# Kernel tuning notes

Hardware: AMD Instinct MI355X
Metric: run time of the kernel (lower is better)

## Reference

```python
import jax, jax.numpy as jnp
from jax import lax
import numpy as np

STRIDE = 2
EXT_PAD = (2, 2)  # computed in __init__: (total_pad - inter_pad)//2 split symmetrically


def setup_inputs() -> dict:
    key = jax.random.key(0)
    k1, k2, k3 = jax.random.split(key, 3)
    x = jax.random.normal(k1, (32, 256, 32, 32), dtype=jnp.float32)
    # Conv kernel in OIHW layout: [out_chs, in_chs, kh, kw]
    W = jax.random.normal(k2, (128, 256, 4, 4), dtype=jnp.float32) * 0.05
    b = jax.random.normal(k3, (128,), dtype=jnp.float32) * 0.01
    return {"x": x, "W": W, "b": b}


def reference(x, W, b):
    # _Interpad: insert (stride-1) zeros between every pair of adjacent spatial
    # elements (not after the last one): new_size = (size-1)*stride + 1.
    B, C, H, Wd = x.shape
    s = STRIDE
    stuffed = jnp.zeros((B, C, (H - 1) * s + 1, (Wd - 1) * s + 1), dtype=x.dtype)
    stuffed = stuffed.at[:, :, ::s, ::s].set(x)
    # external zero padding
    p = EXT_PAD
    padded = jnp.pad(stuffed, ((0, 0), (0, 0), p, p))
    # standard (cross-correlation) conv, stride 1, dilation 1, valid padding
    y = lax.conv_general_dilated(
        padded, W,
        window_strides=(1, 1),
        padding='VALID',
        rhs_dilation=(1, 1),
        dimension_numbers=('NCHW', 'OIHW', 'NCHW'),
    )
    return y + b[None, :, None, None]
```

## Files before the change

kernel.cpp:

```cpp
#include <hip/hip_runtime.h>


typedef float  f32x4  __attribute__((ext_vector_type(4)));
typedef short  short8 __attribute__((ext_vector_type(8)));
typedef unsigned short ushort4v __attribute__((ext_vector_type(4)));
typedef unsigned short ushort8v __attribute__((ext_vector_type(8)));

__device__ __forceinline__ unsigned short f2bf(float f) {
    unsigned u = __builtin_bit_cast(unsigned, f);
    u += 0x7fffu + ((u >> 16) & 1u);
    return (unsigned short)(u >> 16);
}

__device__ __forceinline__ void ld_lds16(const unsigned short* g, unsigned short* l) {
    __builtin_amdgcn_global_load_lds(
        (const __attribute__((address_space(1))) unsigned int*)g,
        (__attribute__((address_space(3))) unsigned int*)l,
        16, 0, 0);
}

#define XP_U 288
#define XP_G 9792
#define XP_N 313344
#define WP_G 8192
#define WP_PI 262144

__global__ __launch_bounds__(256) void prepack_w2(const float* __restrict__ W,
                                                  unsigned short* __restrict__ wp) {
    int t = blockIdx.x * 256 + threadIdx.x;
    int o = t >> 8, c = t & 255;
    int g = c >> 3, c8 = c & 7;
    const float4* src = (const float4*)(W + (size_t)(o * 256 + c) * 16);
    float4 q0 = src[0], q1 = src[1], q2 = src[2], q3 = src[3];
    float rows[4][4] = {{q0.x,q0.y,q0.z,q0.w},{q1.x,q1.y,q1.z,q1.w},
                        {q2.x,q2.y,q2.z,q2.w},{q3.x,q3.y,q3.z,q3.w}};
    #pragma unroll
    for (int pi = 0; pi < 2; ++pi)
    #pragma unroll
    for (int pj = 0; pj < 2; ++pj)
    #pragma unroll
    for (int du = 0; du < 2; ++du)
    #pragma unroll
    for (int dv = 0; dv < 2; ++dv)
        wp[pi*WP_PI + g*WP_G + pj*4096 + (du*2+dv)*1024 + o*8 + c8] =
            f2bf(rows[pi+2*du][pj+2*dv]);
}

__global__ __launch_bounds__(256) void prepack_x(const float* __restrict__ x,
                                                 unsigned short* __restrict__ xp) {
    __shared__ unsigned short xt[256 * 32];
    const int tid = threadIdx.x;
    const int up  = blockIdx.x;
    const int n   = blockIdx.y;
    const bool interior = (up >= 1 && up <= 32);

    if (interior) {
        const int u = up - 1;
        #pragma unroll
        for (int k = 0; k < 8; ++k) {
            int idx4 = tid + k * 256;
            int c = idx4 >> 3, v4 = idx4 & 7;
            float4 val = *(const float4*)(x + ((size_t)(n*256 + c)*32 + u)*32 + v4*4);
            ushort4v s = { f2bf(val.x), f2bf(val.y), f2bf(val.z), f2bf(val.w) };
            *(ushort4v*)&xt[c*32 + v4*4] = s;
        }
        __syncthreads();
    }

    #pragma unroll
    for (int s = 0; s < 5; ++s) {
        int id = tid + s * 256;
        if (id < 1152) {
            int g = id / 36, vp = id % 36;
            ushort8v o8 = {0,0,0,0,0,0,0,0};
            if (interior && vp >= 1 && vp <= 32) {
                #pragma unroll
                for (int e = 0; e < 8; ++e)
                    o8[e] = xt[(g*8 + e)*32 + (vp - 1)];
            }
            *(ushort8v*)&xp[(size_t)n*XP_N + g*XP_G + up*XP_U + vp*8] = o8;
        }
    }
}

__global__ __launch_bounds__(256, 4) void tconv_main(
    const unsigned short* __restrict__ xp,
    const unsigned short* __restrict__ wp,
    const float* __restrict__ bias,
    float* __restrict__ out)
{
    __shared__ __align__(16) unsigned short lds[16384];

    const int tid  = threadIdx.x;
    const int lane = tid & 63;
    const int w    = tid >> 6;
    const int pjw  = w >> 1;
    const int half = w & 1;
    const int lg   = lane >> 4;
    const int ln   = lane & 15;
    const int du   = lg >> 1, dv = lg & 1;

    const int bid = blockIdx.x;
    const int wg  = (bid & 7) * 128 + (bid >> 3);
    const int n   = wg >> 5;
    const int rem = wg & 31;
    const int aq  = rem >> 2;
    const int pi  = (rem >> 1) & 1;
    const int oh  = rem & 1;
    const int a0  = aq * 4;

    const unsigned short* xpb = xp + (size_t)n * XP_N + (a0 + pi) * XP_U
                              + ((half * 2 + du) * XP_U + (ln + pjw + dv) * 8);
    const unsigned short* wpb = wp + pi * WP_PI + oh * 512;

    const int wfoff = (pjw * 4 + lg) * 512 + ln * 8;

    f32x4 acc[4][4];
    #pragma unroll
    for (int i = 0; i < 4; ++i)
        #pragma unroll
        for (int jj = 0; jj < 4; ++jj)
            acc[i][jj] = (f32x4){0.f, 0.f, 0.f, 0.f};

    short8 xA[4], xB[4];

#define STAGE_W(P, BUF)                                                      \
    { _Pragma("unroll")                                                      \
      for (int cc_ = 0; cc_ < 2; ++cc_) {                                    \
        const unsigned short* ws_ = wpb + (size_t)(2*(P) + cc_) * WP_G;      \
        unsigned short* wd_ = (unsigned short*)lds + (BUF)*8192 + cc_*4096;  \
        _Pragma("unroll")                                                    \
        for (int s_ = 0; s_ < 2; ++s_) {                                     \
            int r_ = w * 2 + s_;                                             \
            ld_lds16(ws_ + r_ * 1024 + lane * 8,                             \
                     wd_ + r_ * 512 + lane * 8); } } }

#define LOAD_X(CH, XS)                                                      \
    { const unsigned short* xs_ = xpb + (size_t)(CH) * XP_G;                 \
      XS[0] = *(const short8*)(xs_);                                         \
      XS[1] = *(const short8*)(xs_ + 128);                                   \
      XS[2] = *(const short8*)(xs_ + XP_U);                                  \
      XS[3] = *(const short8*)(xs_ + XP_U + 128); }

#define MFMA_CHUNK(BUF, CC, XS)                                              \
    { const unsigned short* wb_ = (unsigned short*)lds + (BUF)*8192          \
                                  + (CC)*4096 + wfoff;                       \
      __builtin_amdgcn_s_setprio(1);                                        \
      _Pragma("unroll")                                                      \
      for (int i_ = 0; i_ < 4; ++i_) {                                       \
          short8 av_ = *(const short8*)&wb_[i_ * 128];                       \
          _Pragma("unroll")                                                  \
          for (int jj_ = 0; jj_ < 4; ++jj_)                                  \
              acc[i_][jj_] = __builtin_amdgcn_mfma_f32_16x16x32_bf16(        \
                  av_, XS[jj_], acc[i_][jj_], 0, 0, 0);                      \
      }                                                                      \
      __builtin_amdgcn_s_setprio(0); }

#define PHASE_HDR()                                                          \
    __builtin_amdgcn_sched_barrier(0);                                       \
    asm volatile("s_waitcnt vmcnt(8)" ::: "memory");                         \
    __builtin_amdgcn_s_barrier();                                            \
    __builtin_amdgcn_sched_barrier(0);

#define PHASE_FULL(CUR, P)                                                   \
    {                                                                        \
        PHASE_HDR();                                                         \
        STAGE_W((P) + 1, (CUR) ^ 1);                                         \
        __builtin_amdgcn_sched_barrier(0);                                   \
        MFMA_CHUNK(CUR, 0, xA);                                              \
        LOAD_X(2 * (P) + 2, xA);                                             \
        MFMA_CHUNK(CUR, 1, xB);                                              \
        LOAD_X(2 * (P) + 3, xB);                                             \
    }

    STAGE_W(0, 0);
    __builtin_amdgcn_sched_barrier(0);
    LOAD_X(0, xA);
    LOAD_X(1, xB);

    for (int pp = 0; pp < 14; pp += 2) {
        PHASE_FULL(0, pp);
        PHASE_FULL(1, pp + 1);
    }
    PHASE_FULL(0, 14);
    PHASE_HDR();
    MFMA_CHUNK(1, 0, xA);
    MFMA_CHUNK(1, 1, xB);

#undef PHASE_FULL
#undef PHASE_HDR
#undef MFMA_CHUNK
#undef LOAD_X
#undef STAGE_W

    __syncthreads();

    float* epi = (float*)lds;
    #pragma unroll
    for (int i = 0; i < 4; ++i) {
        __syncthreads();
        f32x4 bv = *(const f32x4*)&bias[oh * 64 + i * 16 + lg * 4];
        #pragma unroll
        for (int jj = 0; jj < 4; ++jj) {
            int ar = half * 2 + (jj >> 1);
            int b  = (jj & 1) * 16 + ln;
            #pragma unroll
            for (int r = 0; r < 4; ++r)
                epi[((r * 4 + lg) * 8 + ar * 2 + pjw) * 33 + b] = acc[i][jj][r] + bv[r];
        }
        __syncthreads();
        #pragma unroll
        for (int k = 0; k < 4; ++k) {
            int f    = tid + k * 256;
            int row  = f >> 4;
            int q    = f & 15;
            float2 A = *(const float2*)&epi[(row * 2 + 0) * 33 + q * 2];
            float2 B = *(const float2*)&epi[(row * 2 + 1) * 33 + q * 2];
            float4 v = { A.x, B.x, A.y, B.y };
            int olp   = row >> 2;
            int o     = oh * 64 + i * 16 + ((olp & 3) << 2) + (olp >> 2);
            int i_out = 2 * (a0 + (row & 3)) + pi;
            *(float4*)&out[(((size_t)n * 128 + o) * 64 + i_out) * 64 + q * 4] = v;
        }
    }
}

__global__ __launch_bounds__(256) void prepack_w(const float* __restrict__ W,
                                                 unsigned short* __restrict__ Wp) {
    int t = blockIdx.x * 256 + threadIdx.x;
    int o = t >> 8, c = t & 255;
    const float4* src = (const float4*)(W + (size_t)(o * 256 + c) * 16);
    float4 q0 = src[0], q1 = src[1], q2 = src[2], q3 = src[3];
    float rows[4][4] = {{q0.x,q0.y,q0.z,q0.w},{q1.x,q1.y,q1.z,q1.w},
                        {q2.x,q2.y,q2.z,q2.w},{q3.x,q3.y,q3.z,q3.w}};
    #pragma unroll
    for (int pi = 0; pi < 2; ++pi)
    #pragma unroll
    for (int pj = 0; pj < 2; ++pj)
    #pragma unroll
    for (int du = 0; du < 2; ++du)
    #pragma unroll
    for (int dv = 0; dv < 2; ++dv)
        Wp[((((pi*2+pj)*4 + du*2+dv)*128 + o)*256) + c] = f2bf(rows[pi+2*du][pj+2*dv]);
}

template<bool PRE>
__global__ __launch_bounds__(512, 2) void tconv_mfma(
    const float* __restrict__ x, const float* __restrict__ W,
    const unsigned short* __restrict__ Wp, const float* __restrict__ bias,
    float* __restrict__ out)
{
    __shared__ __align__(16) unsigned short xsh[2][9 * 34 * 8];
    __shared__ __align__(16) unsigned short wsh[2][2 * 4 * 128 * 8];

    const int tid = threadIdx.x;
    const int bid = blockIdx.x;
    const int pi  = bid & 1;
    const int aq  = (bid >> 1) & 3;
    const int n   = bid >> 3;
    const int a0  = aq * 8;
    const int u0  = a0 + pi - 1;

    const int l   = tid & 63;
    const int w   = tid >> 6;
    const int pjw = w >> 2;
    const int q   = w & 3;
    const int lg  = l >> 4;
    const int ln  = l & 15;

    const int sv = tid & 31;
    const int sg = tid >> 5;

    f32x4 acc[8][4];
    #pragma unroll
    for (int i = 0; i < 8; ++i)
        #pragma unroll
        for (int jj = 0; jj < 4; ++jj)
            acc[i][jj] = (f32x4){0.f, 0.f, 0.f, 0.f};

    float    xv[5];
    ushort4v wv[4];
    float4   wa[2], wb[2];

    auto stage_load = [&](int ch) {
        const int c0 = ch * 8;
        #pragma unroll
        for (int s = 0; s < 5; ++s) {
            int p = sg * 5 + s;
            if (p < 72) {
                int c = p & 7, rr = p >> 3;
                int u = u0 + rr;
                xv[s] = ((unsigned)u < 32u)
                      ? x[((n*256 + c0 + c)*32 + u)*32 + sv] : 0.f;
            }
        }
        if (PRE) {
            #pragma unroll
            for (int k = 0; k < 4; ++k) {
                int uu = tid + k * 512;
                int chalf = uu & 1, o = (uu >> 1) & 127;
                int sub = (uu >> 8) & 3, pjq = (uu >> 10) & 1;
                wv[k] = *(const ushort4v*)&Wp[(((pi*2 + pjq)*4 + sub)*128 + o)*256
                                              + c0 + chalf*4];
            }
        } else {
            #pragma unroll
            for (int k = 0; k < 2; ++k) {
                int pr = tid + k * 512;
                int o = pr >> 3, c = pr & 7;
                const float* base = W + ((o*256 + c0 + c) << 4) + pi*4;
                wa[k] = *(const float4*)base;
                wb[k] = *(const float4*)(base + 8);
            }
        }
    };

    auto stage_write = [&](int buf) {
        #pragma unroll
        for (int s = 0; s < 5; ++s) {
            int p = sg * 5 + s;
            if (p < 72) {
                int c = p & 7, rr = p >> 3;
                xsh[buf][(rr*34 + sv + 1)*8 + c] = f2bf(xv[s]);
            }
        }
        if (tid < 144) {
            int pr = tid >> 1;
            int rr = pr >> 3, c = pr & 7;
            int cw = (tid & 1) * 33;
            xsh[buf][(rr*34 + cw)*8 + c] = 0;
        }
        if (PRE) {
            #pragma unroll
            for (int k = 0; k < 4; ++k) {
                int uu = tid + k * 512;
                int chalf = uu & 1, o = (uu >> 1) & 127;
                int sub = (uu >> 8) & 3, pjq = (uu >> 10) & 1;
                *(ushort4v*)&wsh[buf][(((pjq*4 + sub)*128 + o)*8) + chalf*4] = wv[k];
            }
        } else {
            #pragma unroll
            for (int k = 0; k < 2; ++k) {
                int pr = tid + k * 512;
                int o = pr >> 3, c = pr & 7;
                float ra[4] = {wa[k].x, wa[k].y, wa[k].z, wa[k].w};
                float rb[4] = {wb[k].x, wb[k].y, wb[k].z, wb[k].w};
                #pragma unroll
                for (int pj2 = 0; pj2 < 2; ++pj2)
                #pragma unroll
                for (int duu = 0; duu < 2; ++duu)
                #pragma unroll
                for (int dvv = 0; dvv < 2; ++dvv) {
                    float val = duu ? rb[pj2 + 2*dvv] : ra[pj2 + 2*dvv];
                    wsh[buf][(((pj2*4 + duu*2 + dvv)*128 + o)*8) + c] = f2bf(val);
                }
            }
        }
    };

    stage_load(0);
    stage_write(0);
    __syncthreads();

    for (int ch = 0; ch < 32; ++ch) {
        const int cur = ch & 1;
        if (ch + 1 < 32) stage_load(ch + 1);

        short8 bfr[4];
        #pragma unroll
        for (int jj = 0; jj < 4; ++jj) {
            int arow = q*2 + (jj >> 1);
            int b    = (jj & 1)*16 + ln;
            int rr   = arow + (lg >> 1);
            int cw   = b + pjw + (lg & 1);
            bfr[jj]  = *(const short8*)&xsh[cur][(rr*34 + cw)*8];
        }
        #pragma unroll
        for (int i = 0; i < 8; ++i) {
            short8 av = *(const short8*)&wsh[cur][((pjw*4 + lg)*128 + i*16 + ln)*8];
            #pragma unroll
            for (int jj = 0; jj < 4; ++jj)
                acc[i][jj] = __builtin_amdgcn_mfma_f32_16x16x32_bf16(
                                 av, bfr[jj], acc[i][jj], 0, 0, 0);
        }

        if (ch + 1 < 32) stage_write(cur ^ 1);
        __syncthreads();
    }

    #pragma unroll
    for (int i = 0; i < 8; ++i) {
        const f32x4 bv = *(const f32x4*)&bias[i*16 + lg*4];
        #pragma unroll
        for (int jj = 0; jj < 4; ++jj) {
            int arow  = q*2 + (jj >> 1);
            int b     = (jj & 1)*16 + ln;
            int i_out = 2*(a0 + arow) + pi;
            int j_out = 2*b + pjw;
            int o0    = i*16 + lg*4;
            int base  = ((n*128 + o0)*64 + i_out)*64 + j_out;
            #pragma unroll
            for (int r = 0; r < 4; ++r)
                out[base + r*4096] = acc[i][jj][r] + bv[r];
        }
    }
}

extern "C" void kernel_launch(void* const* d_in, const int* in_sizes, int n_in,
                              void* d_out, int out_size, void* d_ws, size_t ws_size,
                              hipStream_t stream) {
    const float* x    = (const float*)d_in[0];
    const float* W    = (const float*)d_in[1];
    const float* bias = (const float*)d_in[2];
    float* out        = (float*)d_out;

    const size_t wp2_bytes = (size_t)2 * WP_PI * 2;
    const size_t xp_bytes  = (size_t)32 * XP_N * 2;
    if (ws_size >= wp2_bytes + xp_bytes) {
        unsigned short* wp2 = (unsigned short*)d_ws;
        unsigned short* xpp = (unsigned short*)((char*)d_ws + wp2_bytes);
        prepack_w2<<<128, 256, 0, stream>>>(W, wp2);
        prepack_x<<<dim3(34, 32), 256, 0, stream>>>(x, xpp);
        tconv_main<<<1024, 256, 0, stream>>>(xpp, wp2, bias, out);
    } else if (ws_size >= (size_t)4*4*128*256*2) {
        unsigned short* Wp = (unsigned short*)d_ws;
        prepack_w<<<128, 256, 0, stream>>>(W, Wp);
        tconv_mfma<true><<<256, 512, 0, stream>>>(x, W, Wp, bias, out);
    } else {
        tconv_mfma<false><<<256, 512, 0, stream>>>(x, W, nullptr, bias, out);
    }
}
```

Before: 57.79 us.

## Split K across two wave groups in main conv kernel and merge prepack kernels

Fuses the weight and input prepack kernels into one launch, so there is one fewer kernel launch. The main transposed-conv kernel goes from 256 to 512 threads per block, and two groups of four waves each handle half of the channel reduction. This halves the serial pipeline length per wave. The partial sums are combined through LDS in the epilogue before bias is added and results are stored. Weight LDS rows are padded (528 stride) to reduce bank conflicts. The cost is double the LDS per block and an extra reduction round with more barriers in the epilogue.

```diff
diff --git a/kernel.cpp b/kernel.cpp
--- a/kernel.cpp
+++ b/kernel.cpp
@@ -24,34 +24,41 @@
 #define XP_N 313344
 #define WP_G 8192
 #define WP_PI 262144
-
-__global__ __launch_bounds__(256) void prepack_w2(const float* __restrict__ W,
-                                                  unsigned short* __restrict__ wp) {
-    int t = blockIdx.x * 256 + threadIdx.x;
-    int o = t >> 8, c = t & 255;
-    int g = c >> 3, c8 = c & 7;
-    const float4* src = (const float4*)(W + (size_t)(o * 256 + c) * 16);
-    float4 q0 = src[0], q1 = src[1], q2 = src[2], q3 = src[3];
-    float rows[4][4] = {{q0.x,q0.y,q0.z,q0.w},{q1.x,q1.y,q1.z,q1.w},
-                        {q2.x,q2.y,q2.z,q2.w},{q3.x,q3.y,q3.z,q3.w}};
-    #pragma unroll
-    for (int pi = 0; pi < 2; ++pi)
-    #pragma unroll
-    for (int pj = 0; pj < 2; ++pj)
-    #pragma unroll
-    for (int du = 0; du < 2; ++du)
-    #pragma unroll
-    for (int dv = 0; dv < 2; ++dv)
-        wp[pi*WP_PI + g*WP_G + pj*4096 + (du*2+dv)*1024 + o*8 + c8] =
-            f2bf(rows[pi+2*du][pj+2*dv]);
-}
-
-__global__ __launch_bounds__(256) void prepack_x(const float* __restrict__ x,
-                                                 unsigned short* __restrict__ xp) {
+#define WROW 528
+#define WCH  4224
+#define WGRP 8448
+#define WBUF 16896
+
+__global__ __launch_bounds__(256) void prepack_all(
+    const float* __restrict__ x, const float* __restrict__ W,
+    unsigned short* __restrict__ wp, unsigned short* __restrict__ xpp)
+{
+    const int tid = threadIdx.x;
+    if (blockIdx.x >= 34) {
+        int wid = (blockIdx.x - 34) * 32 + blockIdx.y;
+        int t = wid * 256 + tid;
+        int o = t >> 8, c = t & 255;
+        int g = c >> 3, c8 = c & 7;
+        const float4* src = (const float4*)(W + (size_t)(o * 256 + c) * 16);
+        float4 q0 = src[0], q1 = src[1], q2 = src[2], q3 = src[3];
+        float rows[4][4] = {{q0.x,q0.y,q0.z,q0.w},{q1.x,q1.y,q1.z,q1.w},
+                            {q2.x,q2.y,q2.z,q2.w},{q3.x,q3.y,q3.z,q3.w}};
+        #pragma unroll
+        for (int pi = 0; pi < 2; ++pi)
+        #pragma unroll
+        for (int pj = 0; pj < 2; ++pj)
+        #pragma unroll
+        for (int du = 0; du < 2; ++du)
+        #pragma unroll
+        for (int dv = 0; dv < 2; ++dv)
+            wp[pi*WP_PI + g*WP_G + pj*4096 + (du*2+dv)*1024 + o*8 + c8] =
+                f2bf(rows[pi+2*du][pj+2*dv]);
+        return;
+    }
+
     __shared__ unsigned short xt[256 * 32];
-    const int tid = threadIdx.x;
-    const int up  = blockIdx.x;
-    const int n   = blockIdx.y;
+    const int up = blockIdx.x;
+    const int n  = blockIdx.y;
     const bool interior = (up >= 1 && up <= 32);
 
     if (interior) {
@@ -78,24 +85,26 @@
                 for (int e = 0; e < 8; ++e)
                     o8[e] = xt[(g*8 + e)*32 + (vp - 1)];
             }
-            *(ushort8v*)&xp[(size_t)n*XP_N + g*XP_G + up*XP_U + vp*8] = o8;
-        }
-    }
-}
-
-__global__ __launch_bounds__(256, 4) void tconv_main(
+            *(ushort8v*)&xpp[(size_t)n*XP_N + g*XP_G + up*XP_U + vp*8] = o8;
+        }
+    }
+}
+
+__global__ __launch_bounds__(512, 4) void tconv_main(
     const unsigned short* __restrict__ xp,
     const unsigned short* __restrict__ wp,
     const float* __restrict__ bias,
     float* __restrict__ out)
 {
-    __shared__ __align__(16) unsigned short lds[16384];
+    __shared__ __align__(16) unsigned short lds[33792];
 
     const int tid  = threadIdx.x;
     const int lane = tid & 63;
     const int w    = tid >> 6;
-    const int pjw  = w >> 1;
-    const int half = w & 1;
+    const int kg   = w >> 2;
+    const int sw   = w & 3;
+    const int pjw  = sw >> 1;
+    const int half = sw & 1;
     const int lg   = lane >> 4;
     const int ln   = lane & 15;
     const int du   = lg >> 1, dv = lg & 1;
@@ -110,10 +119,10 @@
     const int a0  = aq * 4;
 
     const unsigned short* xpb = xp + (size_t)n * XP_N + (a0 + pi) * XP_U
-                              + ((half * 2 + du) * XP_U + (ln + pjw + dv) * 8);
-    const unsigned short* wpb = wp + pi * WP_PI + oh * 512;
-
-    const int wfoff = (pjw * 4 + lg) * 512 + ln * 8;
+                              + ((half * 2 + du) * XP_U + (ln + pjw + dv) * 8)
+                              + (size_t)(kg * 16) * XP_G;
+    const unsigned short* wpb = wp + pi * WP_PI + oh * 512
+                              + (size_t)(kg * 16) * WP_G;
 
     f32x4 acc[4][4];
     #pragma unroll
@@ -126,16 +135,17 @@
 
 #define STAGE_W(P, BUF)                                                      \
     { _Pragma("unroll")                                                      \
-      for (int cc_ = 0; cc_ < 2; ++cc_) {                                    \
-        const unsigned short* ws_ = wpb + (size_t)(2*(P) + cc_) * WP_G;      \
-        unsigned short* wd_ = (unsigned short*)lds + (BUF)*8192 + cc_*4096;  \
-        _Pragma("unroll")                                                    \
-        for (int s_ = 0; s_ < 2; ++s_) {                                     \
-            int r_ = w * 2 + s_;                                             \
-            ld_lds16(ws_ + r_ * 1024 + lane * 8,                             \
-                     wd_ + r_ * 512 + lane * 8); } } }
-
-#define LOAD_X(CH, XS)                                                      \
+      for (int s_ = 0; s_ < 4; ++s_) {                                       \
+          int slot_ = sw * 4 + s_;                                           \
+          int cc_   = slot_ >> 3;                                            \
+          int pjs_  = slot_ & 7;                                             \
+          const unsigned short* src_ = wpb + (size_t)(2*(P) + cc_) * WP_G    \
+                  + (pjs_ >> 2) * 4096 + (pjs_ & 3) * 1024 + lane * 8;       \
+          unsigned short* dst_ = lds + (BUF) * WBUF + kg * WGRP              \
+                  + cc_ * WCH + pjs_ * WROW + lane * 8;                      \
+          ld_lds16(src_, dst_); } }
+
+#define LOAD_X(CH, XS)                                                       \
     { const unsigned short* xs_ = xpb + (size_t)(CH) * XP_G;                 \
       XS[0] = *(const short8*)(xs_);                                         \
       XS[1] = *(const short8*)(xs_ + 128);                                   \
@@ -143,9 +153,9 @@
       XS[3] = *(const short8*)(xs_ + XP_U + 128); }
 
 #define MFMA_CHUNK(BUF, CC, XS)                                              \
-    { const unsigned short* wb_ = (unsigned short*)lds + (BUF)*8192          \
-                                  + (CC)*4096 + wfoff;                       \
-      __builtin_amdgcn_s_setprio(1);                                        \
+    { const unsigned short* wb_ = lds + (BUF) * WBUF + kg * WGRP             \
+                                  + (CC) * WCH + (pjw * 4 + lg) * WROW + ln * 8; \
+      __builtin_amdgcn_s_setprio(1);                                         \
       _Pragma("unroll")                                                      \
       for (int i_ = 0; i_ < 4; ++i_) {                                       \
           short8 av_ = *(const short8*)&wb_[i_ * 128];                       \
@@ -178,11 +188,11 @@
     LOAD_X(0, xA);
     LOAD_X(1, xB);
 
-    for (int pp = 0; pp < 14; pp += 2) {
+    for (int pp = 0; pp < 6; pp += 2) {
         PHASE_FULL(0, pp);
         PHASE_FULL(1, pp + 1);
     }
-    PHASE_FULL(0, 14);
+    PHASE_FULL(0, 6);
     PHASE_HDR();
     MFMA_CHUNK(1, 0, xA);
     MFMA_CHUNK(1, 1, xB);
@@ -193,25 +203,35 @@
 #undef LOAD_X
 #undef STAGE_W
 
-    __syncthreads();
-
-    float* epi = (float*)lds;
+    float* epi  = (float*)lds;
+    float* part = (float*)lds + 4224;
+    const int pidx = (sw * 64 + lane) * 20;
     #pragma unroll
     for (int i = 0; i < 4; ++i) {
         __syncthreads();
-        f32x4 bv = *(const f32x4*)&bias[oh * 64 + i * 16 + lg * 4];
-        #pragma unroll
-        for (int jj = 0; jj < 4; ++jj) {
-            int ar = half * 2 + (jj >> 1);
-            int b  = (jj & 1) * 16 + ln;
-            #pragma unroll
-            for (int r = 0; r < 4; ++r)
-                epi[((r * 4 + lg) * 8 + ar * 2 + pjw) * 33 + b] = acc[i][jj][r] + bv[r];
+        if (kg == 1) {
+            #pragma unroll
+            for (int jj = 0; jj < 4; ++jj)
+                *(f32x4*)&part[pidx + jj * 4] = acc[i][jj];
         }
         __syncthreads();
-        #pragma unroll
-        for (int k = 0; k < 4; ++k) {
-            int f    = tid + k * 256;
+        if (kg == 0) {
+            f32x4 bv = *(const f32x4*)&bias[oh * 64 + i * 16 + lg * 4];
+            #pragma unroll
+            for (int jj = 0; jj < 4; ++jj) {
+                int ar = half * 2 + (jj >> 1);
+                int b  = (jj & 1) * 16 + ln;
+                f32x4 pv = *(const f32x4*)&part[pidx + jj * 4];
+                #pragma unroll
+                for (int r = 0; r < 4; ++r)
+                    epi[((r * 4 + lg) * 8 + ar * 2 + pjw) * 33 + b] =
+                        acc[i][jj][r] + pv[r] + bv[r];
+            }
+        }
+        __syncthreads();
+        #pragma unroll
+        for (int k = 0; k < 2; ++k) {
+            int f    = tid + k * 512;
             int row  = f >> 4;
             int q    = f & 15;
             float2 A = *(const float2*)&epi[(row * 2 + 0) * 33 + q * 2];
@@ -419,9 +439,8 @@
     if (ws_size >= wp2_bytes + xp_bytes) {
         unsigned short* wp2 = (unsigned short*)d_ws;
         unsigned short* xpp = (unsigned short*)((char*)d_ws + wp2_bytes);
-        prepack_w2<<<128, 256, 0, stream>>>(W, wp2);
-        prepack_x<<<dim3(34, 32), 256, 0, stream>>>(x, xpp);
-        tconv_main<<<1024, 256, 0, stream>>>(xpp, wp2, bias, out);
+        prepack_all<<<dim3(38, 32), 256, 0, stream>>>(x, W, wp2, xpp);
+        tconv_main<<<1024, 512, 0, stream>>>(xpp, wp2, bias, out);
     } else if (ws_size >= (size_t)4*4*128*256*2) {
         unsigned short* Wp = (unsigned short*)d_ws;
         prepack_w<<<128, 256, 0, stream>>>(W, Wp);
```

After: 56.29 us. 1.03x faster.
